# Kernel tuning notes

Hardware: AMD Instinct MI355X
Metric: run time of the kernel (lower is better)

The kernel has to match this reference:

```python
import jax, jax.numpy as jnp
import numpy as np

B, H, W, C = 32, 112, 112, 192
K = 7  # spatial attention conv kernel size


def setup_inputs() -> dict:
    key = jax.random.key(0)
    k1, k2 = jax.random.split(key)
    x = jax.random.normal(k1, (B, H, W, C), dtype=jnp.float32)
    # he_normal init for 7x7 conv with 2 input channels, 1 output channel (HWIO)
    fan_in = K * K * 2
    conv_w = jax.random.normal(k2, (K, K, 2, 1), dtype=jnp.float32) * jnp.sqrt(2.0 / fan_in)
    return {"x": x, "conv_w": conv_w}


def reference(x, conv_w):
    # channel-wise reductions: [B,H,W,1] each
    avg_out = jnp.mean(x, axis=-1, keepdims=True)
    max_out = jnp.max(x, axis=-1, keepdims=True)
    concat = jnp.concatenate([avg_out, max_out], axis=-1)  # [B,H,W,2]
    # 7x7 conv, stride 1, SAME padding, no bias -> [B,H,W,1]
    att = jax.lax.conv_general_dilated(
        concat, conv_w,
        window_strides=(1, 1), padding="SAME",
        dimension_numbers=("NHWC", "HWIO", "NHWC"),
    )
    att = jax.nn.sigmoid(att)
    return x * att  # broadcast multiply back onto full feature map
```

## Files before the change

kernel.cpp:

```cpp
#include <hip/hip_runtime.h>
#include <math.h>

#define B_ 32
#define H_ 112
#define W_ 112
#define C_ 192
#define NPOS (B_*H_*W_)
#define C4 (C_/4)
#define HALO 3
#define SW (W_ + 2*HALO)

typedef float nf4 __attribute__((ext_vector_type(4)));

__global__ __launch_bounds__(256) void reduce_kernel(const float* __restrict__ x,
                                                     float2* __restrict__ ws2) {
    const int wave = threadIdx.x >> 6;
    const int lane = threadIdx.x & 63;
    const int sub  = lane & 15;
    const int p = blockIdx.x * 16 + wave * 4 + (lane >> 4);

    const float4* xp = (const float4*)(x + (size_t)p * C_);
    float4 v0 = xp[sub];
    float4 v1 = xp[sub + 16];
    float4 v2 = xp[sub + 32];
    float s = (v0.x + v0.y + v0.z + v0.w)
            + (v1.x + v1.y + v1.z + v1.w)
            + (v2.x + v2.y + v2.z + v2.w);
    float m = fmaxf(fmaxf(fmaxf(v0.x, v0.y), fmaxf(v0.z, v0.w)),
              fmaxf(fmaxf(fmaxf(v1.x, v1.y), fmaxf(v1.z, v1.w)),
                    fmaxf(fmaxf(v2.x, v2.y), fmaxf(v2.z, v2.w))));
    #pragma unroll
    for (int off = 8; off > 0; off >>= 1) {
        s += __shfl_xor(s, off);
        m = fmaxf(m, __shfl_xor(m, off));
    }
    if (sub == 0) {
        float2 r;
        r.x = s * (1.0f / (float)C_);
        r.y = m;
        ws2[p] = r;
    }
}

__global__ __launch_bounds__(256) void fused_kernel(const float* __restrict__ x,
                                                    const float2* __restrict__ ws2,
                                                    const float* __restrict__ w,
                                                    float* __restrict__ out) {
    __shared__ float2 sm[7][SW];
    __shared__ float  sw[98];
    __shared__ float  satt[W_];

    const int tid = threadIdx.x;
    const int rb = (B_ * H_ - 1) - (int)blockIdx.x;
    const int b  = rb / H_;
    const int y  = rb - b * H_;

    if (tid < 98) sw[tid] = w[tid];

    const float2* wsb = ws2 + (size_t)b * (H_ * W_);
    for (int idx = tid; idx < 7 * SW; idx += 256) {
        const int r   = idx / SW;
        const int col = idx - r * SW;
        const int yy  = y + r - HALO;
        const int xx  = col - HALO;
        float2 v = make_float2(0.0f, 0.0f);
        if (yy >= 0 && yy < H_ && xx >= 0 && xx < W_)
            v = wsb[yy * W_ + xx];
        sm[r][col] = v;
    }
    __syncthreads();

    if (tid < W_) {
        float acc = 0.0f;
        #pragma unroll
        for (int ky = 0; ky < 7; ++ky) {
            #pragma unroll
            for (int kx = 0; kx < 7; ++kx) {
                float2 am = sm[ky][tid + kx];
                acc = fmaf(am.x, sw[(ky * 7 + kx) * 2 + 0], acc);
                acc = fmaf(am.y, sw[(ky * 7 + kx) * 2 + 1], acc);
            }
        }
        satt[tid] = 1.0f / (1.0f + __expf(-acc));
    }
    __syncthreads();

    const size_t row4 = ((size_t)b * H_ + y) * W_ * C4;
    const nf4* xr = (const nf4*)x + row4;
    nf4* orow = (nf4*)out + row4;
    #pragma unroll
    for (int k = 0; k < (W_ * C4) / 256; ++k) {
        const int f4  = tid + k * 256;
        const int pos = f4 / C4;
        nf4 v = __builtin_nontemporal_load(&xr[f4]);
        v = v * satt[pos];
        __builtin_nontemporal_store(v, &orow[f4]);
    }
}

extern "C" void kernel_launch(void* const* d_in, const int* in_sizes, int n_in,
                              void* d_out, int out_size, void* d_ws, size_t ws_size,
                              hipStream_t stream) {
    const float* x = (const float*)d_in[0];
    const float* w = (const float*)d_in[1];
    float* out = (float*)d_out;

    float2* ws2 = (float2*)d_ws;

    reduce_kernel<<<NPOS / 16, 256, 0, stream>>>(x, ws2);

    fused_kernel<<<B_ * H_, 256, 0, stream>>>(x, ws2, w, out);
}
```

Before: 150.7 us.

## Fuse channel reduction into row-tiled attention kernel, dropping workspace pass

Removes the separate reduce kernel and workspace. Each block now handles an 8-row tile, recomputing mean/max for its rows plus a 3-row halo directly from x in shared memory, then does the 7x7 conv and multiply. This removes a kernel launch and the workspace round trip, but re-reads halo rows (about 75% extra reduce traffic) and relies on caches for the second read of the tile. It also uses fewer, larger blocks and switches the x load in the multiply to a normal cached load.

```diff
diff --git a/kernel.cpp b/kernel.cpp
--- a/kernel.cpp
+++ b/kernel.cpp
@@ -5,95 +5,92 @@
 #define H_ 112
 #define W_ 112
 #define C_ 192
-#define NPOS (B_*H_*W_)
 #define C4 (C_/4)
+#define R_ 8
+#define TILES (H_/R_)
 #define HALO 3
+#define SR (R_ + 2*HALO)
 #define SW (W_ + 2*HALO)
+#define NT_ 512
 
 typedef float nf4 __attribute__((ext_vector_type(4)));
 
-__global__ __launch_bounds__(256) void reduce_kernel(const float* __restrict__ x,
-                                                     float2* __restrict__ ws2) {
-    const int wave = threadIdx.x >> 6;
-    const int lane = threadIdx.x & 63;
-    const int sub  = lane & 15;
-    const int p = blockIdx.x * 16 + wave * 4 + (lane >> 4);
-
-    const float4* xp = (const float4*)(x + (size_t)p * C_);
-    float4 v0 = xp[sub];
-    float4 v1 = xp[sub + 16];
-    float4 v2 = xp[sub + 32];
-    float s = (v0.x + v0.y + v0.z + v0.w)
-            + (v1.x + v1.y + v1.z + v1.w)
-            + (v2.x + v2.y + v2.z + v2.w);
-    float m = fmaxf(fmaxf(fmaxf(v0.x, v0.y), fmaxf(v0.z, v0.w)),
-              fmaxf(fmaxf(fmaxf(v1.x, v1.y), fmaxf(v1.z, v1.w)),
-                    fmaxf(fmaxf(v2.x, v2.y), fmaxf(v2.z, v2.w))));
-    #pragma unroll
-    for (int off = 8; off > 0; off >>= 1) {
-        s += __shfl_xor(s, off);
-        m = fmaxf(m, __shfl_xor(m, off));
-    }
-    if (sub == 0) {
-        float2 r;
-        r.x = s * (1.0f / (float)C_);
-        r.y = m;
-        ws2[p] = r;
-    }
-}
-
-__global__ __launch_bounds__(256) void fused_kernel(const float* __restrict__ x,
-                                                    const float2* __restrict__ ws2,
+__global__ __launch_bounds__(512) void fused_kernel(const float* __restrict__ x,
                                                     const float* __restrict__ w,
                                                     float* __restrict__ out) {
-    __shared__ float2 sm[7][SW];
+    __shared__ float2 sm[SR][SW];
     __shared__ float  sw[98];
-    __shared__ float  satt[W_];
+    __shared__ float  satt[R_ * W_];
 
     const int tid = threadIdx.x;
-    const int rb = (B_ * H_ - 1) - (int)blockIdx.x;
-    const int b  = rb / H_;
-    const int y  = rb - b * H_;
+    const int b   = blockIdx.x / TILES;
+    const int t   = blockIdx.x - b * TILES;
+    const int y0  = t * R_;
 
     if (tid < 98) sw[tid] = w[tid];
+    for (int i = tid; i < SR * SW; i += NT_)
+        ((float2*)sm)[i] = make_float2(0.0f, 0.0f);
+    __syncthreads();
 
-    const float2* wsb = ws2 + (size_t)b * (H_ * W_);
-    for (int idx = tid; idx < 7 * SW; idx += 256) {
-        const int r   = idx / SW;
-        const int col = idx - r * SW;
-        const int yy  = y + r - HALO;
-        const int xx  = col - HALO;
-        float2 v = make_float2(0.0f, 0.0f);
-        if (yy >= 0 && yy < H_ && xx >= 0 && xx < W_)
-            v = wsb[yy * W_ + xx];
-        sm[r][col] = v;
+    const int lane  = tid & 63;
+    const int sub   = lane & 15;
+    const int pbase = (tid >> 6) * 4 + (lane >> 4);
+    for (int r = 0; r < SR; ++r) {
+        const int yy = y0 + r - HALO;
+        if (yy < 0 || yy >= H_) continue;
+        const float* xrow = x + (size_t)(b * H_ + yy) * W_ * C_;
+        #pragma unroll
+        for (int i = 0; i < 4; ++i) {
+            const int pos = i * 32 + pbase;
+            if (pos < W_) {
+                const float4* xp = (const float4*)(xrow + (size_t)pos * C_);
+                float4 v0 = xp[sub];
+                float4 v1 = xp[sub + 16];
+                float4 v2 = xp[sub + 32];
+                float s = (v0.x + v0.y + v0.z + v0.w)
+                        + (v1.x + v1.y + v1.z + v1.w)
+                        + (v2.x + v2.y + v2.z + v2.w);
+                float m0 = fmaxf(fmaxf(v0.x, v0.y), fmaxf(v0.z, v0.w));
+                float m1 = fmaxf(fmaxf(v1.x, v1.y), fmaxf(v1.z, v1.w));
+                float m2 = fmaxf(fmaxf(v2.x, v2.y), fmaxf(v2.z, v2.w));
+                float m  = fmaxf(m0, fmaxf(m1, m2));
+                #pragma unroll
+                for (int off = 8; off > 0; off >>= 1) {
+                    s += __shfl_xor(s, off);
+                    m = fmaxf(m, __shfl_xor(m, off));
+                }
+                if (sub == 0)
+                    sm[r][HALO + pos] = make_float2(s * (1.0f / (float)C_), m);
+            }
+        }
     }
     __syncthreads();
 
-    if (tid < W_) {
+    for (int idx = tid; idx < R_ * W_; idx += NT_) {
+        const int rr  = idx / W_;
+        const int col = idx - rr * W_;
         float acc = 0.0f;
         #pragma unroll
         for (int ky = 0; ky < 7; ++ky) {
             #pragma unroll
             for (int kx = 0; kx < 7; ++kx) {
-                float2 am = sm[ky][tid + kx];
+                float2 am = sm[rr + ky][col + kx];
                 acc = fmaf(am.x, sw[(ky * 7 + kx) * 2 + 0], acc);
                 acc = fmaf(am.y, sw[(ky * 7 + kx) * 2 + 1], acc);
             }
         }
-        satt[tid] = 1.0f / (1.0f + __expf(-acc));
+        satt[idx] = 1.0f / (1.0f + __expf(-acc));
     }
     __syncthreads();
 
-    const size_t row4 = ((size_t)b * H_ + y) * W_ * C4;
-    const nf4* xr = (const nf4*)x + row4;
-    nf4* orow = (nf4*)out + row4;
-    #pragma unroll
-    for (int k = 0; k < (W_ * C4) / 256; ++k) {
-        const int f4  = tid + k * 256;
-        const int pos = f4 / C4;
-        nf4 v = __builtin_nontemporal_load(&xr[f4]);
-        v = v * satt[pos];
+    const size_t base4 = (size_t)(b * H_ + y0) * W_ * C4;
+    const nf4* xr   = (const nf4*)x + base4;
+    nf4*       orow = (nf4*)out + base4;
+    #pragma unroll 4
+    for (int k = 0; k < (R_ * W_ * C4) / NT_; ++k) {
+        const int f4 = tid + k * NT_;
+        nf4 v = xr[f4];
+        v = v * satt[f4 / C4];
         __builtin_nontemporal_store(v, &orow[f4]);
     }
 }
@@ -104,10 +101,5 @@
     const float* x = (const float*)d_in[0];
     const float* w = (const float*)d_in[1];
     float* out = (float*)d_out;
-
-    float2* ws2 = (float2*)d_ws;
-
-    reduce_kernel<<<NPOS / 16, 256, 0, stream>>>(x, ws2);
-
-    fused_kernel<<<B_ * H_, 256, 0, stream>>>(x, ws2, w, out);
+    fused_kernel<<<B_ * TILES, NT_, 0, stream>>>(x, w, out);
 }
```

After: 179.8 us. 1.19x slower.

## Chunk batch into cache-sized pieces so the second pass over x hits cache

Applied to the files above, without the earlier changes.

Splits the two-kernel pipeline into four batch chunks of 8 images. Each chunk runs its reduction and then its conv-multiply pass, so the second read of x can come from the last-level cache instead of HBM. The conv-multiply kernel now handles half rows (56 columns) per block, which doubles the block count. The x load is now a normal load rather than non-temporal, so the data can stay cached. The cost is eight kernel launches instead of two, plus one more serialization point per chunk.

```diff
diff --git a/kernel.cpp b/kernel.cpp
--- a/kernel.cpp
+++ b/kernel.cpp
@@ -5,19 +5,21 @@
 #define H_ 112
 #define W_ 112
 #define C_ 192
-#define NPOS (B_*H_*W_)
 #define C4 (C_/4)
+#define CHB 8
+#define NCHUNK (B_/CHB)
+#define CPOS (CHB*H_*W_)
 #define HALO 3
-#define SW (W_ + 2*HALO)
 
 typedef float nf4 __attribute__((ext_vector_type(4)));
 
 __global__ __launch_bounds__(256) void reduce_kernel(const float* __restrict__ x,
-                                                     float2* __restrict__ ws2) {
+                                                     float2* __restrict__ ws2,
+                                                     int p0) {
     const int wave = threadIdx.x >> 6;
     const int lane = threadIdx.x & 63;
     const int sub  = lane & 15;
-    const int p = blockIdx.x * 16 + wave * 4 + (lane >> 4);
+    const int p = p0 + blockIdx.x * 16 + wave * 4 + (lane >> 4);
 
     const float4* xp = (const float4*)(x + (size_t)p * C_);
     float4 v0 = xp[sub];
@@ -26,9 +28,10 @@
     float s = (v0.x + v0.y + v0.z + v0.w)
             + (v1.x + v1.y + v1.z + v1.w)
             + (v2.x + v2.y + v2.z + v2.w);
-    float m = fmaxf(fmaxf(fmaxf(v0.x, v0.y), fmaxf(v0.z, v0.w)),
-              fmaxf(fmaxf(fmaxf(v1.x, v1.y), fmaxf(v1.z, v1.w)),
-                    fmaxf(fmaxf(v2.x, v2.y), fmaxf(v2.z, v2.w))));
+    float m0 = fmaxf(fmaxf(v0.x, v0.y), fmaxf(v0.z, v0.w));
+    float m1 = fmaxf(fmaxf(v1.x, v1.y), fmaxf(v1.z, v1.w));
+    float m2 = fmaxf(fmaxf(v2.x, v2.y), fmaxf(v2.z, v2.w));
+    float m  = fmaxf(m0, fmaxf(m1, m2));
     #pragma unroll
     for (int off = 8; off > 0; off >>= 1) {
         s += __shfl_xor(s, off);
@@ -42,35 +45,37 @@
     }
 }
 
-__global__ __launch_bounds__(256) void fused_kernel(const float* __restrict__ x,
-                                                    const float2* __restrict__ ws2,
-                                                    const float* __restrict__ w,
-                                                    float* __restrict__ out) {
-    __shared__ float2 sm[7][SW];
+__global__ __launch_bounds__(256) void convmul_kernel(const float* __restrict__ x,
+                                                      const float2* __restrict__ ws2,
+                                                      const float* __restrict__ w,
+                                                      float* __restrict__ out,
+                                                      int row0) {
+    __shared__ float2 sm[7][64];
     __shared__ float  sw[98];
-    __shared__ float  satt[W_];
+    __shared__ float  satt[56];
 
-    const int tid = threadIdx.x;
-    const int rb = (B_ * H_ - 1) - (int)blockIdx.x;
-    const int b  = rb / H_;
-    const int y  = rb - b * H_;
+    const int tid  = threadIdx.x;
+    const int rowg = row0 + ((int)blockIdx.x >> 1);
+    const int x0   = ((int)blockIdx.x & 1) * 56;
+    const int b    = rowg / H_;
+    const int y    = rowg - b * H_;
 
     if (tid < 98) sw[tid] = w[tid];
 
     const float2* wsb = ws2 + (size_t)b * (H_ * W_);
-    for (int idx = tid; idx < 7 * SW; idx += 256) {
-        const int r   = idx / SW;
-        const int col = idx - r * SW;
-        const int yy  = y + r - HALO;
-        const int xx  = col - HALO;
+    for (int i = tid; i < 7 * 62; i += 256) {
+        const int r  = i / 62;
+        const int c  = i - r * 62;
+        const int yy = y + r - HALO;
+        const int xx = x0 + c - HALO;
         float2 v = make_float2(0.0f, 0.0f);
         if (yy >= 0 && yy < H_ && xx >= 0 && xx < W_)
             v = wsb[yy * W_ + xx];
-        sm[r][col] = v;
+        sm[r][c] = v;
     }
     __syncthreads();
 
-    if (tid < W_) {
+    if (tid < 56) {
         float acc = 0.0f;
         #pragma unroll
         for (int ky = 0; ky < 7; ++ky) {
@@ -85,16 +90,13 @@
     }
     __syncthreads();
 
-    const size_t row4 = ((size_t)b * H_ + y) * W_ * C4;
-    const nf4* xr = (const nf4*)x + row4;
-    nf4* orow = (nf4*)out + row4;
-    #pragma unroll
-    for (int k = 0; k < (W_ * C4) / 256; ++k) {
-        const int f4  = tid + k * 256;
-        const int pos = f4 / C4;
-        nf4 v = __builtin_nontemporal_load(&xr[f4]);
-        v = v * satt[pos];
-        __builtin_nontemporal_store(v, &orow[f4]);
+    const size_t base4 = (size_t)rowg * (W_ * C4) + (size_t)x0 * C4;
+    const nf4* xr   = (const nf4*)x + base4;
+    nf4*       orow = (nf4*)out + base4;
+    for (int f = tid; f < 56 * C4; f += 256) {
+        nf4 v = xr[f];
+        v = v * satt[f / C4];
+        __builtin_nontemporal_store(v, &orow[f]);
     }
 }
 
@@ -104,10 +106,11 @@
     const float* x = (const float*)d_in[0];
     const float* w = (const float*)d_in[1];
     float* out = (float*)d_out;
-
     float2* ws2 = (float2*)d_ws;
 
-    reduce_kernel<<<NPOS / 16, 256, 0, stream>>>(x, ws2);
-
-    fused_kernel<<<B_ * H_, 256, 0, stream>>>(x, ws2, w, out);
+    for (int c = 0; c < NCHUNK; ++c) {
+        reduce_kernel<<<CPOS / 16, 256, 0, stream>>>(x, ws2, c * CPOS);
+        convmul_kernel<<<CHB * H_ * 2, 256, 0, stream>>>(x, ws2, w, out,
+                                                         c * CHB * H_);
+    }
 }
```

Result: slower. 158.8 us (+5.4%).
